# Kernel optimization log

Hardware: AMD Instinct MI355X
Metric: run time of the kernel (lower is better)

Reference implementation:

```python
import jax, jax.numpy as jnp
import numpy as np
import math

H = 12          # num_attention_heads
DH = 64         # attention_head_size
D = H * DH      # hidden_size = 768
LN_EPS = 1e-5
GAUSS_W = 0.3989422804014327
WIDS = [None, 0.1, 1.0, 5.0]


def gauss_weight(L, wid):
    # faithful to generate_gauss_weight: row-normalized Gaussian bump per query pos
    center = (jnp.arange(L, dtype=jnp.float32) / L)[:, None]       # (L,1)
    pos = jnp.linspace(0.0, 1.0, L, dtype=jnp.float32)[None, :]    # (1,L)
    width = max(wid, 0.01) / 9.0                                   # static python scalar
    g = (GAUSS_W / width) * jnp.exp(-(pos - center) ** 2 / (2.0 * width * width))
    return g / jnp.max(g, axis=-1, keepdims=True)                  # (L,L)


def layer_norm(x, g, b):
    mu = jnp.mean(x, axis=-1, keepdims=True)
    var = jnp.mean((x - mu) ** 2, axis=-1, keepdims=True)
    return (x - mu) * jax.lax.rsqrt(var + LN_EPS) * g + b


def bert_attention(x, mask, qkv_w, qkv_b, out_w, out_b, ln_g, ln_b, wid):
    # x: (N,L,D); mask: (N,L,L); qkv_w: (3,D,D); qkv_b: (3,D)
    N, L, _ = x.shape

    def heads(t):  # (N,L,D) -> (N,H,L,DH)
        return t.reshape(N, L, H, DH).transpose(0, 2, 1, 3)

    q = heads(x @ qkv_w[0] + qkv_b[0])
    k = heads(x @ qkv_w[1] + qkv_b[1])
    v = heads(x @ qkv_w[2] + qkv_b[2])

    scores = jnp.einsum('nhqd,nhkd->nhqk', q, k) / math.sqrt(DH)   # (N,H,L,L)
    if wid is not None:
        scores = scores * gauss_weight(L, wid)[None, None]          # multiplicative GMM mask
    scores = scores + (1.0 - mask[:, None, :, :]) * -10000.0
    probs = jax.nn.softmax(scores, axis=-1)                         # dropout = identity (eval)
    ctx = jnp.einsum('nhqk,nhkd->nhqd', probs, v)                   # (N,H,L,DH)
    ctx = ctx.transpose(0, 2, 1, 3).reshape(N, L, D)

    proj = ctx @ out_w + out_b
    return layer_norm(proj + x, ln_g, ln_b)


def setup_inputs() -> dict:
    key = jax.random.key(0)
    ks = jax.random.split(key, 4)
    N, L = 4, 1024
    s = 0.02
    return {
        'input_tensor': jax.random.normal(ks[0], (N, L, D), dtype=jnp.float32),
        'attention_mask': jnp.ones((N, L, L), dtype=jnp.float32),
        'qkv_w': jax.random.normal(ks[1], (4, 3, D, D), dtype=jnp.float32) * s,
        'qkv_b': jnp.zeros((4, 3, D), dtype=jnp.float32),
        'out_w': jax.random.normal(ks[2], (4, D, D), dtype=jnp.float32) * s,
        'out_b': jnp.zeros((4, D), dtype=jnp.float32),
        'ln_g': jnp.ones((4, D), dtype=jnp.float32),
        'ln_b': jnp.zeros((4, D), dtype=jnp.float32),
    }


def reference(input_tensor, attention_mask, qkv_w, qkv_b, out_w, out_b, ln_g, ln_b):
    # pure_block=False path: 4 parallel GMM-masked attention branches, averaged
    outs = [
        bert_attention(input_tensor, attention_mask,
                       qkv_w[i], qkv_b[i], out_w[i], out_b[i], ln_g[i], ln_b[i], WIDS[i])
        for i in range(4)
    ]
    return jnp.mean(jnp.stack(outs, axis=-1), axis=-1)
```

## Files before the change

kernel.cpp:

```cpp
#include <hip/hip_runtime.h>
#include <hip/hip_bf16.h>

#define NB 4
#define LQ 1024
#define NH 12
#define DHD 64
#define DM 768
#define MTOT (NB*LQ)
#define L2E 1.4426950408889634f
#define SMB 11.541560327111708f
#define CFAR 3.3546262790251185e-4f

typedef __attribute__((ext_vector_type(4))) float f32x4;
typedef __attribute__((ext_vector_type(8))) short bf16x8;
typedef __attribute__((ext_vector_type(4))) short short4v;
typedef unsigned short u16;

#if __has_builtin(__builtin_amdgcn_exp2f)
#define EXP2(x) __builtin_amdgcn_exp2f(x)
#else
#define EXP2(x) __expf((x) * 0.6931471805599453f)
#endif

__device__ __forceinline__ u16 f2bf(float f){
  union { float f; unsigned int i; } v; v.f = f;
  unsigned int r = v.i + 0x7FFFu + ((v.i >> 16) & 1u);
  return (u16)(r >> 16);
}
__device__ __forceinline__ float bf2f(u16 u){
  union { unsigned int i; float f; } v; v.i = ((unsigned int)u) << 16;
  return v.f;
}
__device__ __forceinline__ unsigned cvt_pk_bf16(float lo, float hi){
  unsigned r;
  asm("v_cvt_pk_bf16_f32 %0, %1, %2" : "=v"(r) : "v"(lo), "v"(hi));
  return r;
}

typedef const __attribute__((address_space(1))) void* gas_t;
typedef __attribute__((address_space(3))) void* las_t;
__device__ __forceinline__ void gload16(const void* g, void* l){
  __builtin_amdgcn_global_load_lds((gas_t)g, (las_t)l, 16, 0, 0);
}

__global__ void k_cvt_x(const float* __restrict__ x, u16* __restrict__ xb){
  int i = (blockIdx.x * 256 + threadIdx.x) * 4;
  float4 v = *reinterpret_cast<const float4*>(x + i);
  short4v o;
  o[0] = (short)f2bf(v.x); o[1] = (short)f2bf(v.y);
  o[2] = (short)f2bf(v.z); o[3] = (short)f2bf(v.w);
  *reinterpret_cast<short4v*>(xb + i) = o;
}

__global__ void k_wt(const float* __restrict__ qkv_w, const float* __restrict__ out_w,
                     u16* __restrict__ wt){
  int mat = blockIdx.z;
  const float* W = (mat < 12) ? (qkv_w + (size_t)mat*DM*DM)
                              : (out_w + (size_t)(mat-12)*DM*DM);
  __shared__ float tile[32][33];
  int j0 = blockIdx.x*32, k0 = blockIdx.y*32;
  int tx = threadIdx.x, ty = threadIdx.y;
  #pragma unroll
  for (int i=0;i<4;i++)
    tile[ty + i*8][tx] = W[(size_t)(k0 + ty + i*8)*DM + j0 + tx];
  __syncthreads();
  u16* dst = wt + (size_t)mat*DM*DM;
  int tid = ty*32 + tx;
  int jj = tid >> 3, kq = tid & 7;
  short4v pk;
  #pragma unroll
  for (int t=0;t<4;t++) pk[t] = (short)f2bf(tile[kq*4 + t][jj]);
  *reinterpret_cast<short4v*>(&dst[(size_t)(j0 + jj)*DM + k0 + kq*4]) = pk;
}

__global__ void k_maskchk(const float* __restrict__ mask, unsigned* __restrict__ flags){
  int qt = blockIdx.x, kt = blockIdx.y, n = blockIdx.z;
  const float* M = mask + ((size_t)(n*LQ) + qt*64)*LQ + kt*64;
  int tid = threadIdx.x;
  int r = tid >> 2, c4 = (tid & 3) * 16;
  int ok = 1;
  #pragma unroll
  for (int j=0;j<4;j++){
    float4 v = *reinterpret_cast<const float4*>(M + (size_t)r*LQ + c4 + j*4);
    ok &= (v.x==1.f) & (v.y==1.f) & (v.z==1.f) & (v.w==1.f);
  }
  __shared__ int sok[4];
  unsigned long long bal = __ballot(ok);
  if ((tid & 63) == 0) sok[tid>>6] = (bal == 0xFFFFFFFFFFFFFFFFull) ? 1 : 0;
  __syncthreads();
  if (tid == 0) flags[((size_t)n*16 + qt)*16 + kt] = sok[0] & sok[1] & sok[2] & sok[3];
}

__global__ __launch_bounds__(256) void k_vsum(const u16* __restrict__ qkvws, float* __restrict__ ps){
  const int nh = blockIdx.x;
  const int b  = blockIdx.y;
  const size_t blk = (size_t)NB*NH*LQ*DHD;
  const u16* Vt = qkvws + (size_t)(b*3+2)*blk + (size_t)nh*DHD*LQ;
  const int tid = threadIdx.x;
  const int dh = tid >> 2, c = tid & 3;
  float* psb = ps + ((size_t)(b*48 + nh)*17)*64;
  float acc = 0.f;
  for (int kt = 0; kt < 16; ++kt){
    if (c == 0) psb[kt*64 + dh] = acc;
    bf16x8 v0 = *reinterpret_cast<const bf16x8*>(&Vt[(size_t)dh*LQ + kt*64 + c*16]);
    bf16x8 v1 = *reinterpret_cast<const bf16x8*>(&Vt[(size_t)dh*LQ + kt*64 + c*16 + 8]);
    float s = 0.f;
    #pragma unroll
    for (int j=0;j<8;j++) s += bf2f((u16)v0[j]) + bf2f((u16)v1[j]);
    s += __shfl_xor(s, 1);
    s += __shfl_xor(s, 2);
    acc += s;
  }
  if (c == 0) psb[16*64 + dh] = acc;
}

__device__ __forceinline__ void gemm_tile(const u16* __restrict__ Ag,
                                          const u16* __restrict__ Bg,
                                          u16* a_lds, u16* b_lds, f32x4 acc[4][4])
{
  const int tid = threadIdx.x, lane = tid & 63, w = tid >> 6;
  const int wr = (w >> 1) * 64, wc = (w & 1) * 64;
  const int rl = lane & 15, q4 = lane >> 4;
  const int lrow = lane >> 3;
  const int lseg = (lane & 7) ^ lrow;
  for (int k0 = 0; k0 < DM; k0 += 64) {
    __syncthreads();
    #pragma unroll
    for (int cc = 0; cc < 4; ++cc) {
      int c = w*4 + cc;
      const u16* ga = Ag + (size_t)(c*8 + lrow)*DM + k0 + lseg*8;
      const u16* gb = Bg + (size_t)(c*8 + lrow)*DM + k0 + lseg*8;
      gload16(ga, a_lds + c*512);
      gload16(gb, b_lds + c*512);
    }
    __syncthreads();
    #pragma unroll
    for (int half = 0; half < 2; ++half) {
      bf16x8 af[4], bfr[4];
      #pragma unroll
      for (int f = 0; f < 4; ++f) {
        int ra = wr + f*16 + rl;
        int rb = wc + f*16 + rl;
        int ta = (half*4 + q4) ^ (ra & 7);
        int tb = (half*4 + q4) ^ (rb & 7);
        af[f]  = *reinterpret_cast<const bf16x8*>(&a_lds[ra*64 + ta*8]);
        bfr[f] = *reinterpret_cast<const bf16x8*>(&b_lds[rb*64 + tb*8]);
      }
      #pragma unroll
      for (int mf=0; mf<4; ++mf)
        #pragma unroll
        for (int nf=0; nf<4; ++nf)
          acc[mf][nf] = __builtin_amdgcn_mfma_f32_16x16x32_bf16(af[mf], bfr[nf], acc[mf][nf], 0,0,0);
    }
  }
}

__global__ __launch_bounds__(256) void k_qkv(const u16* __restrict__ xb, const u16* __restrict__ wt,
                     const float* __restrict__ qkv_b, u16* __restrict__ qkvws)
{
  __shared__ __align__(16) u16 a_lds[128*64];
  __shared__ __align__(16) u16 b_lds[128*64];
  const int bid = blockIdx.x;
  const int orig = (bid & 7) * 288 + (bid >> 3);
  const int m0 = (orig & 31) * 128;
  const int j0 = ((orig >> 5) % 6) * 128;
  const int mat = orig / 192;
  const int t = mat % 3;
  f32x4 acc[4][4] = {};
  gemm_tile(xb + (size_t)m0*DM, wt + (size_t)mat*DM*DM + (size_t)j0*DM, a_lds, b_lds, acc);

  const int tid = threadIdx.x, lane = tid & 63, w = tid >> 6;
  const int wr = (w >> 1) * 64, wc = (w & 1) * 64;
  const int rl = lane & 15, rg = (lane >> 4) * 4;
  const float sc = (t == 0) ? 0.125f : 1.0f;
  const size_t matbase = (size_t)mat * ((size_t)NB*NH*LQ*DHD);
  #pragma unroll
  for (int nf=0; nf<4; ++nf) {
    int j = j0 + wc + nf*16 + rl;
    float bias = qkv_b[mat*DM + j];
    int h = j >> 6, dh = j & 63;
    #pragma unroll
    for (int mf=0; mf<4; ++mf) {
      int mB = m0 + wr + mf*16 + rg;
      int n = mB >> 10, l = mB & 1023;
      if (t < 2) {
        #pragma unroll
        for (int i=0;i<4;i++)
          qkvws[matbase + ((size_t)(n*NH + h)*LQ + (l+i))*DHD + dh] = f2bf((acc[mf][nf][i] + bias) * sc);
      } else {
        short4v pk;
        #pragma unroll
        for (int i=0;i<4;i++) pk[i] = (short)f2bf(acc[mf][nf][i] + bias);
        *reinterpret_cast<short4v*>(&qkvws[matbase + ((size_t)(n*NH + h)*DHD + dh)*LQ + l]) = pk;
      }
    }
  }
}

__global__ __launch_bounds__(512) void k_attn(const u16* __restrict__ qkvws, const float* __restrict__ mask,
                      const unsigned* __restrict__ flags, const float* __restrict__ ps,
                      u16* __restrict__ ctx, float c2_1, float c2_2, float c2_3)
{
  __shared__ __align__(16) u16 kv_lds[2][2][64*64];
  __shared__ __align__(16) u16 p_lds[128*64];
  const int bid = blockIdx.x;
  const int orig = (bid & 7) * 192 + (bid >> 3);
  const int qp = orig & 7;
  const int b  = (orig >> 3) & 3;
  const int nh = orig >> 5;
  const int n = nh / NH, h = nh % NH;
  const float c2 = (b==1) ? c2_1 : (b==2) ? c2_2 : c2_3;
  const bool useG = (b != 0);
  const int tid = threadIdx.x, lane = tid & 63, w = tid >> 6;
  const int wl = w & 3, half = w >> 2;
  const int qt = qp*2 + half;
  const int rl = lane & 15, q4 = lane >> 4, kc8 = q4*8, rg = q4*4;
  const int q0 = qt*64 + wl*16;

  const size_t hb = (size_t)(n*NH + h);
  const size_t blk = (size_t)NB*NH*LQ*DHD;
  const u16* Qb = qkvws + (size_t)(b*3+0)*blk + hb*LQ*DHD;
  const u16* Kb = qkvws + (size_t)(b*3+1)*blk + hb*LQ*DHD;
  const u16* Vt = qkvws + (size_t)(b*3+2)*blk + hb*DHD*LQ;
  const float* Mb = mask + (size_t)n*LQ*LQ;

  bf16x8 qf0 = *reinterpret_cast<const bf16x8*>(&Qb[(size_t)(q0+rl)*DHD + kc8]);
  bf16x8 qf1 = *reinterpret_cast<const bf16x8*>(&Qb[(size_t)(q0+rl)*DHD + 32 + kc8]);

  float srun[4] = {0.f,0.f,0.f,0.f};
  float dmin2[4], cq[4];
  f32x4 o[4] = {};
  #pragma unroll
  for (int i=0;i<4;i++){
    int q = q0 + rg + i;
    float c = (float)q * (1.0f/1024.0f);
    float ksf = floorf(c * 1023.0f + 0.5f);
    float dm = ksf * (1.0f/1023.0f) - c;
    cq[i] = c; dmin2[i] = dm*dm;
  }

  int lo_a, hi_a, lo_b, hi_b, ra_a, ra_b;
  {
    int qa = qp*2, qb = qp*2+1;
    int r0 = 1, r1 = 1;
    for (int t = 0; t < 16; ++t){
      r0 &= (flags[((size_t)n*16 + qa)*16 + t] != 0u) ? 1 : 0;
      r1 &= (flags[((size_t)n*16 + qb)*16 + t] != 0u) ? 1 : 0;
    }
    ra_a = r0; ra_b = r1;
    lo_a = 0; hi_a = 16; lo_b = 0; hi_b = 16;
    if (r0){
      if (b == 1){ lo_a = qa>0?qa-1:0; hi_a = qa<15?qa+2:16; }
      else if (b == 2){ lo_a = qa>5?qa-5:0; hi_a = qa<10?qa+6:16; }
    }
    if (r1){
      if (b == 1){ lo_b = qb>0?qb-1:0; hi_b = qb<15?qb+2:16; }
      else if (b == 2){ lo_b = qb>5?qb-5:0; hi_b = qb<10?qb+6:16; }
    }
  }
  const int mylo = half ? lo_b : lo_a;
  const int myhi = half ? hi_b : hi_a;
  const int myrowall = half ? ra_b : ra_a;
  const int blo = lo_a < lo_b ? lo_a : lo_b;
  const int bhi = hi_a > hi_b ? hi_a : hi_b;
  const int mynt = myhi - mylo;

  if (myrowall && mynt < 16){
    const float* psb = ps + ((size_t)(b*48 + nh)*17)*64;
    #pragma unroll
    for (int nf=0; nf<4; ++nf){
      int dh = nf*16 + rl;
      float sfar = psb[16*64 + dh] - psb[myhi*64 + dh] + psb[mylo*64 + dh];
      float fv = CFAR * sfar;
      #pragma unroll
      for (int i=0;i<4;i++) o[nf][i] = fv;
    }
    float sinit = CFAR * (float)(64*(16 - mynt));
    #pragma unroll
    for (int i=0;i<4;i++) srun[i] = sinit;
  }

  const int r8 = tid >> 3;
  const int uu = (tid & 7) ^ (r8 & 7);

  #define STAGE8(buf, kt_) { \
    gload16(Kb + (size_t)((kt_)*64 + r8)*DHD + uu*8, (u16*)kv_lds[buf][0] + tid*8); \
    gload16(Vt + (size_t)r8*LQ + (kt_)*64 + uu*8, (u16*)kv_lds[buf][1] + tid*8); }

  STAGE8(0, blo);
  __syncthreads();

  const int nloop = bhi - blo;
  for (int it = 0; it < nloop; ++it){
    const int kt = blo + it;
    const int cur = it & 1;
    if (it + 1 < nloop) STAGE8(cur^1, kt+1);

    if (kt >= mylo && kt < myhi){
      const bool allones = myrowall || (flags[((size_t)n*16 + qt)*16 + kt] != 0u);
      const u16* kbuf = (const u16*)kv_lds[cur][0];
      const u16* vbuf = (const u16*)kv_lds[cur][1];

      f32x4 sf[4] = {};
      #pragma unroll
      for (int nf=0; nf<4; ++nf){
        int row = nf*16 + rl, sw = (row & 7) << 3;
        bf16x8 kf0 = *reinterpret_cast<const bf16x8*>(&kbuf[row*64 + (kc8 ^ sw)]);
        bf16x8 kf1 = *reinterpret_cast<const bf16x8*>(&kbuf[row*64 + ((32 + kc8) ^ sw)]);
        sf[nf] = __builtin_amdgcn_mfma_f32_16x16x32_bf16(qf0, kf0, sf[nf], 0,0,0);
        sf[nf] = __builtin_amdgcn_mfma_f32_16x16x32_bf16(qf1, kf1, sf[nf], 0,0,0);
      }

      float pv[4][4];
      #pragma unroll
      for (int nf=0; nf<4; ++nf){
        int key = kt*64 + nf*16 + rl;
        float pos = (float)key * (1.0f/1023.0f);
        #pragma unroll
        for (int i=0;i<4;i++){
          float s = sf[nf][i];
          if (useG){
            float d = pos - cq[i];
            float tg = fmaf(-d, d, dmin2[i]);
            s *= EXP2(tg * c2);
          }
          if (!allones){
            int q = q0 + rg + i;
            s = fmaf(1.0f - Mb[(size_t)q*LQ + key], -10000.0f, s);
          }
          float p = EXP2(fmaf(s, L2E, -SMB));
          srun[i] += p;
          pv[nf][i] = p;
        }
      }

      #pragma unroll
      for (int np=0; np<2; ++np)
        #pragma unroll
        for (int i=0;i<4;i++){
          unsigned u = cvt_pk_bf16(pv[np*2][i], pv[np*2+1][i]);
          int row = w*16 + rg + i, sw = (row & 7) << 3;
          p_lds[row*64 + ((np*32 + rl) ^ sw)]      = (u16)(u & 0xffffu);
          p_lds[row*64 + ((np*32 + 16 + rl) ^ sw)] = (u16)(u >> 16);
        }
      asm volatile("s_waitcnt lgkmcnt(0)" ::: "memory");
      __builtin_amdgcn_sched_barrier(0);

      {
        int prow = w*16 + rl, psw = (prow & 7) << 3;
        bf16x8 pa0 = *reinterpret_cast<const bf16x8*>(&p_lds[prow*64 + (kc8 ^ psw)]);
        bf16x8 pa1 = *reinterpret_cast<const bf16x8*>(&p_lds[prow*64 + ((32 + kc8) ^ psw)]);
        #pragma unroll
        for (int nf=0; nf<4; ++nf){
          int row = nf*16 + rl, sw = (row & 7) << 3;
          bf16x8 vv0 = *reinterpret_cast<const bf16x8*>(&vbuf[row*64 + (kc8 ^ sw)]);
          bf16x8 vv1 = *reinterpret_cast<const bf16x8*>(&vbuf[row*64 + ((32 + kc8) ^ sw)]);
          o[nf] = __builtin_amdgcn_mfma_f32_16x16x32_bf16(pa0, vv0, o[nf], 0,0,0);
          o[nf] = __builtin_amdgcn_mfma_f32_16x16x32_bf16(pa1, vv1, o[nf], 0,0,0);
        }
      }
    }
    __syncthreads();
  }

  #pragma unroll
  for (int off=1; off<16; off<<=1){
    #pragma unroll
    for (int i=0;i<4;i++) srun[i] += __shfl_xor(srun[i], off);
  }
  #pragma unroll
  for (int i=0;i<4;i++){
    float inv = 1.0f / (srun[i] + 1e-35f);
    int q = q0 + rg + i;
    size_t mrow = ((size_t)(n*LQ + q)) * DM;
    #pragma unroll
    for (int nf=0; nf<4; ++nf){
      int d = h*DHD + nf*16 + rl;
      ctx[(size_t)b*((size_t)MTOT*DM) + mrow + d] = f2bf(o[nf][i] * inv);
    }
  }
  #undef STAGE8
}

__global__ __launch_bounds__(256) void k_proj(const u16* __restrict__ ctx, const u16* __restrict__ wt,
                      const float* __restrict__ out_b, u16* __restrict__ proj)
{
  __shared__ __align__(16) u16 a_lds[128*64];
  __shared__ __align__(16) u16 b_lds[128*64];
  const int bid = blockIdx.x;
  const int orig = (bid & 7) * 96 + (bid >> 3);
  const int m0 = (orig & 31) * 128;
  const int j0 = ((orig >> 5) % 6) * 128;
  const int b = orig / 192;
  f32x4 acc[4][4] = {};
  gemm_tile(ctx + (size_t)b*MTOT*DM + (size_t)m0*DM,
            wt + (size_t)(12+b)*DM*DM + (size_t)j0*DM, a_lds, b_lds, acc);
  const int tid = threadIdx.x, lane = tid & 63, w = tid >> 6;
  const int wr = (w >> 1) * 64, wc = (w & 1) * 64;
  const int rl = lane & 15, rg = (lane >> 4) * 4;
  #pragma unroll
  for (int nf=0; nf<4; ++nf) {
    int j = j0 + wc + nf*16 + rl;
    float bias = out_b[b*DM + j];
    #pragma unroll
    for (int mf=0; mf<4; ++mf) {
      int mB = m0 + wr + mf*16 + rg;
      #pragma unroll
      for (int i=0;i<4;i++)
        proj[((size_t)b*MTOT + (mB+i))*DM + j] = f2bf(acc[mf][nf][i] + bias);
    }
  }
}

__global__ __launch_bounds__(256) void k_ln(const float* __restrict__ x, const u16* __restrict__ proj,
                    const float* __restrict__ ln_g, const float* __restrict__ ln_b,
                    float* __restrict__ out)
{
  const int m = blockIdx.x;
  const int tid = threadIdx.x, lane = tid & 63, w = tid >> 6;
  __shared__ float rb[4][2][4];
  float xr[3], acc[3] = {0.f,0.f,0.f};
  #pragma unroll
  for (int c=0;c<3;c++) xr[c] = x[(size_t)m*DM + tid + c*256];
  float vv[4][3], s1[4], s2[4];
  #pragma unroll
  for (int b=0;b<4;b++){
    s1[b] = 0.f; s2[b] = 0.f;
    #pragma unroll
    for (int c=0;c<3;c++){
      float v = bf2f(proj[((size_t)b*MTOT + m)*DM + tid + c*256]) + xr[c];
      vv[b][c] = v; s1[b] += v; s2[b] += v*v;
    }
  }
  #pragma unroll
  for (int b=0;b<4;b++){
    #pragma unroll
    for (int off=32; off>=1; off>>=1){
      s1[b] += __shfl_xor(s1[b], off);
      s2[b] += __shfl_xor(s2[b], off);
    }
    if (lane == 0){ rb[b][0][w] = s1[b]; rb[b][1][w] = s2[b]; }
  }
  __syncthreads();
  #pragma unroll
  for (int b=0;b<4;b++){
    float S1 = rb[b][0][0]+rb[b][0][1]+rb[b][0][2]+rb[b][0][3];
    float S2 = rb[b][1][0]+rb[b][1][1]+rb[b][1][2]+rb[b][1][3];
    float mu = S1 * (1.0f/768.0f);
    float var = S2 * (1.0f/768.0f) - mu*mu;
    float rs = rsqrtf(var + 1e-5f);
    #pragma unroll
    for (int c=0;c<3;c++){
      int j = tid + c*256;
      acc[c] += 0.25f * ((vv[b][c]-mu)*rs*ln_g[b*DM+j] + ln_b[b*DM+j]);
    }
  }
  #pragma unroll
  for (int c=0;c<3;c++) out[(size_t)m*DM + tid + c*256] = acc[c];
}

extern "C" void kernel_launch(void* const* d_in, const int* in_sizes, int n_in,
                              void* d_out, int out_size, void* d_ws, size_t ws_size,
                              hipStream_t stream)
{
  const float* x     = (const float*)d_in[0];
  const float* mask  = (const float*)d_in[1];
  const float* qkv_w = (const float*)d_in[2];
  const float* qkv_b = (const float*)d_in[3];
  const float* out_w = (const float*)d_in[4];
  const float* out_b = (const float*)d_in[5];
  const float* ln_g  = (const float*)d_in[6];
  const float* ln_b  = (const float*)d_in[7];
  float* out = (float*)d_out;
  char* ws = (char*)d_ws;

  u16* xb        = (u16*)(ws);
  unsigned* flags= (unsigned*)(ws);
  float* ps      = (float*)(ws + 8192);
  u16* wt        = (u16*)(ws + 6291456);
  u16* qkv       = (u16*)(ws + 25165824);
  u16* ctx       = (u16*)(ws + 100663296);
  u16* proj      = (u16*)(ws + 25165824);

  float c2[3];
  const float wid[3] = {0.1f, 1.0f, 5.0f};
  for (int i=0;i<3;i++){
    float wdt = wid[i]/9.0f;
    c2[i] = (1.0f/(2.0f*wdt*wdt)) * L2E;
  }

  k_cvt_x<<<dim3(3072), dim3(256), 0, stream>>>(x, xb);
  k_wt<<<dim3(24,24,16), dim3(32,8), 0, stream>>>(qkv_w, out_w, wt);
  k_qkv<<<dim3(2304), dim3(256), 0, stream>>>(xb, wt, qkv_b, qkv);
  k_vsum<<<dim3(48,4), dim3(256), 0, stream>>>(qkv, ps);
  k_maskchk<<<dim3(16,16,4), dim3(256), 0, stream>>>(mask, flags);
  k_attn<<<dim3(1536), dim3(512), 0, stream>>>(qkv, mask, flags, ps, ctx, c2[0], c2[1], c2[2]);
  k_proj<<<dim3(768), dim3(256), 0, stream>>>(ctx, wt, out_b, proj);
  k_ln<<<dim3(4096), dim3(256), 0, stream>>>(x, proj, ln_g, ln_b, out);
}
```

Baseline: 264.9 us.

## Double-buffer GEMM K-tiles at K=32 and stage epilogue stores through LDS

Replaces the single-buffered 64-wide K loop in the shared GEMM tile with a double-buffered 32-wide K loop. The next tile's global-to-LDS load is issued before computing on the current one, leaving one barrier per iteration. The Q/K and projection epilogues now write the output tile into padded LDS and then emit 16-byte coalesced global stores instead of scattered 2-byte stores. This adds an extra barrier and LDS traffic in the epilogue and halves MFMA work per iteration, which may expose more loop overhead.

```diff
diff --git a/kernel.cpp b/kernel.cpp
--- a/kernel.cpp
+++ b/kernel.cpp
@@ -114,52 +114,52 @@
   if (c == 0) psb[16*64 + dh] = acc;
 }
 
-__device__ __forceinline__ void gemm_tile(const u16* __restrict__ Ag,
-                                          const u16* __restrict__ Bg,
-                                          u16* a_lds, u16* b_lds, f32x4 acc[4][4])
+__device__ __forceinline__ void gemm_tile32(const u16* __restrict__ Ag,
+                                            const u16* __restrict__ Bg,
+                                            u16* smem, f32x4 acc[4][4])
 {
   const int tid = threadIdx.x, lane = tid & 63, w = tid >> 6;
   const int wr = (w >> 1) * 64, wc = (w & 1) * 64;
   const int rl = lane & 15, q4 = lane >> 4;
-  const int lrow = lane >> 3;
-  const int lseg = (lane & 7) ^ lrow;
-  for (int k0 = 0; k0 < DM; k0 += 64) {
+  const int srow = tid >> 2;
+  const int su = (tid & 3) ^ ((srow >> 1) & 3);
+
+  #define QSTG(buf, k0_) { \
+    _Pragma("unroll") \
+    for (int r = 0; r < 2; ++r){ \
+      gload16(Ag + (size_t)(r*64 + srow)*DM + (k0_) + su*8, smem + (buf)*8192 + r*2048 + tid*8); \
+      gload16(Bg + (size_t)(r*64 + srow)*DM + (k0_) + su*8, smem + (buf)*8192 + 4096 + r*2048 + tid*8); \
+    } }
+
+  QSTG(0, 0);
+  __syncthreads();
+  for (int it = 0; it < 24; ++it){
+    const int cur = it & 1;
+    if (it + 1 < 24) QSTG(cur^1, (it+1)*32);
+    const u16* al = smem + cur*8192;
+    const u16* bl = al + 4096;
+    bf16x8 af[4], bfr[4];
+    #pragma unroll
+    for (int f = 0; f < 4; ++f){
+      int ra = wr + f*16 + rl, rb = wc + f*16 + rl;
+      int ua = q4 ^ ((ra >> 1) & 3), ub = q4 ^ ((rb >> 1) & 3);
+      af[f]  = *reinterpret_cast<const bf16x8*>(&al[ra*32 + ua*8]);
+      bfr[f] = *reinterpret_cast<const bf16x8*>(&bl[rb*32 + ub*8]);
+    }
+    #pragma unroll
+    for (int mf=0; mf<4; ++mf)
+      #pragma unroll
+      for (int nf=0; nf<4; ++nf)
+        acc[mf][nf] = __builtin_amdgcn_mfma_f32_16x16x32_bf16(af[mf], bfr[nf], acc[mf][nf], 0,0,0);
     __syncthreads();
-    #pragma unroll
-    for (int cc = 0; cc < 4; ++cc) {
-      int c = w*4 + cc;
-      const u16* ga = Ag + (size_t)(c*8 + lrow)*DM + k0 + lseg*8;
-      const u16* gb = Bg + (size_t)(c*8 + lrow)*DM + k0 + lseg*8;
-      gload16(ga, a_lds + c*512);
-      gload16(gb, b_lds + c*512);
-    }
-    __syncthreads();
-    #pragma unroll
-    for (int half = 0; half < 2; ++half) {
-      bf16x8 af[4], bfr[4];
-      #pragma unroll
-      for (int f = 0; f < 4; ++f) {
-        int ra = wr + f*16 + rl;
-        int rb = wc + f*16 + rl;
-        int ta = (half*4 + q4) ^ (ra & 7);
-        int tb = (half*4 + q4) ^ (rb & 7);
-        af[f]  = *reinterpret_cast<const bf16x8*>(&a_lds[ra*64 + ta*8]);
-        bfr[f] = *reinterpret_cast<const bf16x8*>(&b_lds[rb*64 + tb*8]);
-      }
-      #pragma unroll
-      for (int mf=0; mf<4; ++mf)
-        #pragma unroll
-        for (int nf=0; nf<4; ++nf)
-          acc[mf][nf] = __builtin_amdgcn_mfma_f32_16x16x32_bf16(af[mf], bfr[nf], acc[mf][nf], 0,0,0);
-    }
-  }
+  }
+  #undef QSTG
 }
 
 __global__ __launch_bounds__(256) void k_qkv(const u16* __restrict__ xb, const u16* __restrict__ wt,
                      const float* __restrict__ qkv_b, u16* __restrict__ qkvws)
 {
-  __shared__ __align__(16) u16 a_lds[128*64];
-  __shared__ __align__(16) u16 b_lds[128*64];
+  __shared__ __align__(16) u16 smem[17408];
   const int bid = blockIdx.x;
   const int orig = (bid & 7) * 288 + (bid >> 3);
   const int m0 = (orig & 31) * 128;
@@ -167,27 +167,49 @@
   const int mat = orig / 192;
   const int t = mat % 3;
   f32x4 acc[4][4] = {};
-  gemm_tile(xb + (size_t)m0*DM, wt + (size_t)mat*DM*DM + (size_t)j0*DM, a_lds, b_lds, acc);
+  gemm_tile32(xb + (size_t)m0*DM, wt + (size_t)mat*DM*DM + (size_t)j0*DM, smem, acc);
 
   const int tid = threadIdx.x, lane = tid & 63, w = tid >> 6;
   const int wr = (w >> 1) * 64, wc = (w & 1) * 64;
   const int rl = lane & 15, rg = (lane >> 4) * 4;
   const float sc = (t == 0) ? 0.125f : 1.0f;
   const size_t matbase = (size_t)mat * ((size_t)NB*NH*LQ*DHD);
-  #pragma unroll
-  for (int nf=0; nf<4; ++nf) {
-    int j = j0 + wc + nf*16 + rl;
-    float bias = qkv_b[mat*DM + j];
-    int h = j >> 6, dh = j & 63;
-    #pragma unroll
-    for (int mf=0; mf<4; ++mf) {
-      int mB = m0 + wr + mf*16 + rg;
-      int n = mB >> 10, l = mB & 1023;
-      if (t < 2) {
+  if (t < 2){
+    #pragma unroll
+    for (int nf=0; nf<4; ++nf){
+      int jc = wc + nf*16 + rl;
+      float bias = qkv_b[mat*DM + j0 + jc];
+      #pragma unroll
+      for (int mf=0; mf<4; ++mf){
+        int row = wr + mf*16 + rg;
         #pragma unroll
         for (int i=0;i<4;i++)
-          qkvws[matbase + ((size_t)(n*NH + h)*LQ + (l+i))*DHD + dh] = f2bf((acc[mf][nf][i] + bias) * sc);
-      } else {
+          smem[(row+i)*136 + jc] = f2bf((acc[mf][nf][i] + bias) * sc);
+      }
+    }
+    __syncthreads();
+    const int n = m0 >> 10, l0 = m0 & 1023;
+    const int hbase = j0 >> 6;
+    #pragma unroll
+    for (int jj=0; jj<8; ++jj){
+      int idx = tid + 256*jj;
+      int l = idx >> 4, ch = idx & 15;
+      bf16x8 v = *reinterpret_cast<const bf16x8*>(&smem[l*136 + ch*8]);
+      int hh = hbase + (ch >> 3);
+      int dh0 = (ch & 7) * 8;
+      *reinterpret_cast<bf16x8*>(
+        &qkvws[matbase + ((size_t)(n*NH + hh)*LQ + l0 + l)*DHD + dh0]) = v;
+    }
+  } else {
+    #pragma unroll
+    for (int nf=0; nf<4; ++nf){
+      int j = j0 + wc + nf*16 + rl;
+      float bias = qkv_b[mat*DM + j];
+      int h = j >> 6, dh = j & 63;
+      #pragma unroll
+      for (int mf=0; mf<4; ++mf){
+        int mB = m0 + wr + mf*16 + rg;
+        int n = mB >> 10, l = mB & 1023;
         short4v pk;
         #pragma unroll
         for (int i=0;i<4;i++) pk[i] = (short)f2bf(acc[mf][nf][i] + bias);
@@ -385,30 +407,37 @@
 __global__ __launch_bounds__(256) void k_proj(const u16* __restrict__ ctx, const u16* __restrict__ wt,
                       const float* __restrict__ out_b, u16* __restrict__ proj)
 {
-  __shared__ __align__(16) u16 a_lds[128*64];
-  __shared__ __align__(16) u16 b_lds[128*64];
+  __shared__ __align__(16) u16 smem[17408];
   const int bid = blockIdx.x;
   const int orig = (bid & 7) * 96 + (bid >> 3);
   const int m0 = (orig & 31) * 128;
   const int j0 = ((orig >> 5) % 6) * 128;
   const int b = orig / 192;
   f32x4 acc[4][4] = {};
-  gemm_tile(ctx + (size_t)b*MTOT*DM + (size_t)m0*DM,
-            wt + (size_t)(12+b)*DM*DM + (size_t)j0*DM, a_lds, b_lds, acc);
+  gemm_tile32(ctx + (size_t)b*MTOT*DM + (size_t)m0*DM,
+              wt + (size_t)(12+b)*DM*DM + (size_t)j0*DM, smem, acc);
   const int tid = threadIdx.x, lane = tid & 63, w = tid >> 6;
   const int wr = (w >> 1) * 64, wc = (w & 1) * 64;
   const int rl = lane & 15, rg = (lane >> 4) * 4;
   #pragma unroll
-  for (int nf=0; nf<4; ++nf) {
-    int j = j0 + wc + nf*16 + rl;
-    float bias = out_b[b*DM + j];
-    #pragma unroll
-    for (int mf=0; mf<4; ++mf) {
-      int mB = m0 + wr + mf*16 + rg;
+  for (int nf=0; nf<4; ++nf){
+    int jc = wc + nf*16 + rl;
+    float bias = out_b[b*DM + j0 + jc];
+    #pragma unroll
+    for (int mf=0; mf<4; ++mf){
+      int row = wr + mf*16 + rg;
       #pragma unroll
       for (int i=0;i<4;i++)
-        proj[((size_t)b*MTOT + (mB+i))*DM + j] = f2bf(acc[mf][nf][i] + bias);
-    }
+        smem[(row+i)*136 + jc] = f2bf(acc[mf][nf][i] + bias);
+    }
+  }
+  __syncthreads();
+  #pragma unroll
+  for (int jj=0; jj<8; ++jj){
+    int idx = tid + 256*jj;
+    int l = idx >> 4, ch = idx & 15;
+    bf16x8 v = *reinterpret_cast<const bf16x8*>(&smem[l*136 + ch*8]);
+    *reinterpret_cast<bf16x8*>(&proj[((size_t)b*MTOT + m0 + l)*DM + j0 + ch*8]) = v;
   }
 }
 
```

New measurement: 265.1 us. About the same (+0.1%).
